# Optimization experiments

Measured on AMD Instinct MI355X. Metric: run time of the kernel, lower is better.

Reference implementation:

```python
import jax, jax.numpy as jnp
import numpy as np
from jax import lax

B, T, D = 2048, 300, 40
H = 64          # BasicLSTMCell num_units
D1 = 128        # dense1 units
OUT = 512       # out_dim (num speakers)
FORGET_BIAS = 1.0
BN_EPS = 1e-3   # tf.layers.BatchNormalization default


def setup_inputs() -> dict:
    key = jax.random.key(0)
    ks = jax.random.split(key, 10)
    X = jax.random.normal(ks[0], (B, T, D), dtype=jnp.float32)
    seq_length = jax.random.randint(ks[1], (B,), 1, T + 1).astype(jnp.int32)
    # BasicLSTMCell kernel: [input_dim + H, 4H], gate order i, j, f, o
    lstm_kernel = jax.random.normal(ks[2], (D + H, 4 * H), dtype=jnp.float32) * 0.08
    lstm_bias = jnp.zeros((4 * H,), dtype=jnp.float32)
    W1 = jax.random.normal(ks[3], (H, D1), dtype=jnp.float32) * 0.1
    b1 = jnp.zeros((D1,), dtype=jnp.float32)
    gamma = jnp.ones((D1,), dtype=jnp.float32)
    beta = jnp.zeros((D1,), dtype=jnp.float32)
    moving_mean = jnp.zeros((D1,), dtype=jnp.float32)
    moving_var = jnp.ones((D1,), dtype=jnp.float32)
    W2 = jax.random.normal(ks[4], (D1, OUT), dtype=jnp.float32) * 0.1
    b2 = jnp.zeros((OUT,), dtype=jnp.float32)
    return {"X": X, "seq_length": seq_length,
            "lstm_kernel": lstm_kernel, "lstm_bias": lstm_bias,
            "W1": W1, "b1": b1, "gamma": gamma, "beta": beta,
            "moving_mean": moving_mean, "moving_var": moving_var,
            "W2": W2, "b2": b2}


def reference(X, seq_length, lstm_kernel, lstm_bias, W1, b1, gamma, beta,
              moving_mean, moving_var, W2, b2):
    b = X.shape[0]
    c0 = jnp.zeros((b, H), dtype=X.dtype)
    h0 = jnp.zeros((b, H), dtype=X.dtype)

    def step(carry, x_t):
        c, h = carry
        z = jnp.concatenate([x_t, h], axis=1) @ lstm_kernel + lstm_bias
        i, j, f, o = jnp.split(z, 4, axis=1)
        new_c = c * jax.nn.sigmoid(f + FORGET_BIAS) + jax.nn.sigmoid(i) * jnp.tanh(j)
        new_h = jnp.tanh(new_c) * jax.nn.sigmoid(o)
        return (new_c, new_h), new_h

    _, outs = lax.scan(step, (c0, h0), jnp.swapaxes(X, 0, 1))  # [T, B, H]
    outs = jnp.swapaxes(outs, 0, 1)  # [B, T, H]

    # gather last valid timestep per sample
    idx = (seq_length - 1).astype(jnp.int32)
    final = jnp.take_along_axis(outs, idx[:, None, None], axis=1)[:, 0, :]  # [B, H]

    x = jax.nn.relu(final @ W1 + b1)
    # BatchNorm in inference mode (training=False): use moving statistics
    x = gamma * (x - moving_mean) * lax.rsqrt(moving_var + BN_EPS) + beta
    return jax.nn.softmax(x @ W2 + b2, axis=-1)
```

## Files before the change

### kernel.cpp

```cpp
#include <hip/hip_runtime.h>
#include <stdint.h>

#define TT 300
#define DD 40
#define SB 4
#define AROW 200
#define ABUF (16 * AROW)

typedef __attribute__((ext_vector_type(8))) short short8;
typedef __attribute__((ext_vector_type(4))) float f32x4;

__device__ __forceinline__ ushort f2bf(float f) {
  uint32_t b = __float_as_uint(f);
  b += 0x7FFFu + ((b >> 16) & 1u);
  return (ushort)(b >> 16);
}

__device__ __forceinline__ void bar() {
  asm volatile("s_waitcnt lgkmcnt(0)" ::: "memory");
  __builtin_amdgcn_s_barrier();
  asm volatile("" ::: "memory");
}

__global__ __launch_bounds__(256, 1) void lstm_mfma_kernel(
    const float* __restrict__ X, const int* __restrict__ seqlen,
    const float* __restrict__ Wk, const float* __restrict__ bias,
    float* __restrict__ hfin)
{
  __shared__ ushort wstage[64 * 192];
  __shared__ ushort Ash[2 * ABUF];

  const int tid = threadIdx.x;
  const int wv = tid >> 6, lane = tid & 63;
  const int s0 = blockIdx.x * SB;

  for (int i = tid; i < 2 * ABUF; i += 256) Ash[i] = 0;

  short8 Bf[6][4];
  for (int c = 0; c < 4; ++c) {
    __syncthreads();
    for (int i = tid; i < 64 * 192; i += 256) {
      int cc = i & 63, kp = i >> 6;
      int g = cc >> 4, u = c * 16 + (cc & 15);
      int col = g * 64 + u;
      ushort v = 0;
      if (kp < 40) {
        v = f2bf(Wk[kp * 256 + col]);
      } else if (kp < 42) {
        float bv = bias[col] + ((g == 2) ? 1.0f : 0.0f);
        ushort hi = f2bf(bv);
        v = (kp == 40) ? hi : f2bf(bv - __uint_as_float((uint32_t)hi << 16));
      } else if (kp >= 64) {
        v = f2bf(Wk[(40 + ((kp - 64) >> 1)) * 256 + col]);
      }
      wstage[cc * 192 + kp] = v;
    }
    __syncthreads();
    if (wv == c) {
      #pragma unroll
      for (int kt = 0; kt < 6; ++kt) {
        int kk = kt * 32 + (lane >> 4) * 8;
        #pragma unroll
        for (int g = 0; g < 4; ++g)
          Bf[kt][g] = *reinterpret_cast<const short8*>(
              &wstage[(g * 16 + (lane & 15)) * 192 + kk]);
      }
    }
  }

  const int u = wv * 16 + (lane & 15);
  const int q = lane >> 4;
  const bool act = (q < 2);
  const int sl0 = 2 * q, sl1 = sl0 + 1;
  const int len0 = seqlen[s0 + (sl0 & 3)], len1 = seqlen[s0 + (sl1 & 3)];

  int ml = seqlen[s0 + (lane & 3)];
  #pragma unroll
  for (int off = 1; off < 4; off <<= 1) ml = max(ml, __shfl_xor(ml, off));

  const bool hasX = (tid < SB * DD);
  const int sA = (tid * 205) >> 13, dA = tid - sA * 40;
  const int rA = 4 * (sA >> 1) + (sA & 1);
  const float* pA = X + (size_t)(s0 + sA) * (TT * DD) + dA;
  const int xiA = rA * AROW + dA;

  if (tid < 8) {
    int s = tid & 3, b = tid >> 2;
    int row = 4 * (s >> 1) + (s & 1);
    Ash[b * ABUF + row * AROW + 40] = 0x3F80;
    Ash[b * ABUF + row * AROW + 41] = 0x3F80;
  }
  float xv = 0.f;
  if (hasX) {
    Ash[xiA] = f2bf(pA[0]);
    if (ml > 1) xv = pA[DD];
  }
  __syncthreads();
  pA += 2 * DD;

  float c0 = 0.f, c1 = 0.f, hf0 = 0.f, hf1 = 0.f;
  int rb = 0, wb = ABUF;
  const int afb = (lane & 15) * AROW + q * 8;
  const int hw0 = (q * 4) * AROW + 64 + 2 * u;
  const int hw1 = (q * 4 + 1) * AROW + 64 + 2 * u;

  for (int t = 0; t < ml; ++t) {
    short8 Af[6];
    #pragma unroll
    for (int kt = 0; kt < 6; ++kt)
      Af[kt] = *reinterpret_cast<const short8*>(&Ash[rb + afb + kt * 32]);

    float xn = 0.f;
    if (hasX && t + 2 < ml) { xn = pA[0]; pA += DD; }

    f32x4 zero4 = {0.f, 0.f, 0.f, 0.f};
    f32x4 acc0 = zero4, acc1 = zero4, acc2 = zero4, acc3 = zero4;
    #pragma unroll
    for (int kt = 0; kt < 6; ++kt) {
      acc0 = __builtin_amdgcn_mfma_f32_16x16x32_bf16(Af[kt], Bf[kt][0], acc0, 0, 0, 0);
      acc1 = __builtin_amdgcn_mfma_f32_16x16x32_bf16(Af[kt], Bf[kt][1], acc1, 0, 0, 0);
      acc2 = __builtin_amdgcn_mfma_f32_16x16x32_bf16(Af[kt], Bf[kt][2], acc2, 0, 0, 0);
      acc3 = __builtin_amdgcn_mfma_f32_16x16x32_bf16(Af[kt], Bf[kt][3], acc3, 0, 0, 0);
    }

    if (act) {
      float Ef0 = __expf(-acc2[0]), Ei0 = __expf(-acc0[0]), Ej0 = __expf(2.f * acc1[0]);
      float nc0 = fmaf(c0, __builtin_amdgcn_rcpf(1.f + Ef0),
                       (Ej0 - 1.f) * __builtin_amdgcn_rcpf((1.f + Ei0) * (1.f + Ej0)));
      float En0 = __expf(2.f * fminf(nc0, 44.f)), Eo0 = __expf(-acc3[0]);
      float nh0 = (En0 - 1.f) * __builtin_amdgcn_rcpf((1.f + En0) * (1.f + Eo0));

      float Ef1 = __expf(-acc2[1]), Ei1 = __expf(-acc0[1]), Ej1 = __expf(2.f * acc1[1]);
      float nc1 = fmaf(c1, __builtin_amdgcn_rcpf(1.f + Ef1),
                       (Ej1 - 1.f) * __builtin_amdgcn_rcpf((1.f + Ei1) * (1.f + Ej1)));
      float En1 = __expf(2.f * fminf(nc1, 44.f)), Eo1 = __expf(-acc3[1]);
      float nh1 = (En1 - 1.f) * __builtin_amdgcn_rcpf((1.f + En1) * (1.f + Eo1));

      c0 = nc0; c1 = nc1;
      if (t == len0 - 1) hf0 = nh0;
      if (t == len1 - 1) hf1 = nh1;

      ushort hh0 = f2bf(nh0);
      ushort hl0 = f2bf(nh0 - __uint_as_float((uint32_t)hh0 << 16));
      ushort hh1 = f2bf(nh1);
      ushort hl1 = f2bf(nh1 - __uint_as_float((uint32_t)hh1 << 16));
      *reinterpret_cast<uint32_t*>(&Ash[wb + hw0]) = (uint32_t)hh0 | ((uint32_t)hl0 << 16);
      *reinterpret_cast<uint32_t*>(&Ash[wb + hw1]) = (uint32_t)hh1 | ((uint32_t)hl1 << 16);
    }
    if (hasX && t + 1 < ml) Ash[wb + xiA] = f2bf(xv);

    bar();
    rb ^= ABUF; wb ^= ABUF;
    xv = xn;
  }

  if (act) {
    hfin[(size_t)(s0 + sl0) * 64 + u] = hf0;
    hfin[(size_t)(s0 + sl1) * 64 + u] = hf1;
  }
}

__global__ __launch_bounds__(256, 1) void head_kernel(
    const float* __restrict__ hfin,
    const float* __restrict__ W1, const float* __restrict__ b1,
    const float* __restrict__ gamma, const float* __restrict__ beta,
    const float* __restrict__ mmean, const float* __restrict__ mvar,
    const float* __restrict__ W2, const float* __restrict__ b2,
    float* __restrict__ out)
{
  __shared__ float hl[16 * 64];
  __shared__ float d1t[128 * 20];
  __shared__ float lg[16 * 516];
  const int tid = threadIdx.x;
  const int b0 = blockIdx.x * 16;

  for (int i = tid; i < 16 * 64; i += 256) hl[i] = hfin[(size_t)b0 * 64 + i];
  __syncthreads();

  {
    const int j = tid & 127, sg = tid >> 7;
    float acc[8];
    const float bb = b1[j];
    #pragma unroll
    for (int s = 0; s < 8; ++s) acc[s] = bb;
    for (int k = 0; k < 64; ++k) {
      float w = W1[k * 128 + j];
      #pragma unroll
      for (int s = 0; s < 8; ++s) acc[s] = fmaf(hl[(sg * 8 + s) * 64 + k], w, acc[s]);
    }
    const float ga = gamma[j], be = beta[j], mm = mmean[j];
    const float iv = rsqrtf(mvar[j] + 1e-3f);
    #pragma unroll
    for (int s = 0; s < 8; ++s) {
      float v = fmaxf(acc[s], 0.f);
      d1t[j * 20 + sg * 8 + s] = ga * (v - mm) * iv + be;
    }
  }
  __syncthreads();

  {
    const int cA = tid * 2;
    float accA[16], accB[16];
    const float bA = b2[cA], bB = b2[cA + 1];
    #pragma unroll
    for (int s = 0; s < 16; ++s) { accA[s] = bA; accB[s] = bB; }
    for (int k = 0; k < 128; ++k) {
      const float2 w = *reinterpret_cast<const float2*>(&W2[k * 512 + cA]);
      const f32x4 dq0 = *reinterpret_cast<const f32x4*>(&d1t[k * 20]);
      const f32x4 dq1 = *reinterpret_cast<const f32x4*>(&d1t[k * 20 + 4]);
      const f32x4 dq2 = *reinterpret_cast<const f32x4*>(&d1t[k * 20 + 8]);
      const f32x4 dq3 = *reinterpret_cast<const f32x4*>(&d1t[k * 20 + 12]);
      #pragma unroll
      for (int s = 0; s < 4; ++s) {
        accA[s]      = fmaf(dq0[s], w.x, accA[s]);      accB[s]      = fmaf(dq0[s], w.y, accB[s]);
        accA[s + 4]  = fmaf(dq1[s], w.x, accA[s + 4]);  accB[s + 4]  = fmaf(dq1[s], w.y, accB[s + 4]);
        accA[s + 8]  = fmaf(dq2[s], w.x, accA[s + 8]);  accB[s + 8]  = fmaf(dq2[s], w.y, accB[s + 8]);
        accA[s + 12] = fmaf(dq3[s], w.x, accA[s + 12]); accB[s + 12] = fmaf(dq3[s], w.y, accB[s + 12]);
      }
    }
    #pragma unroll
    for (int s = 0; s < 16; ++s) {
      lg[s * 516 + cA]     = accA[s];
      lg[s * 516 + cA + 1] = accB[s];
    }
  }
  __syncthreads();

  {
    const int w = tid >> 6, lane = tid & 63;
    #pragma unroll
    for (int si = 0; si < 4; ++si) {
      const int s = w * 4 + si;
      float v[8];
      float m = -3.4e38f;
      #pragma unroll
      for (int i = 0; i < 8; ++i) { v[i] = lg[s * 516 + lane + 64 * i]; m = fmaxf(m, v[i]); }
      #pragma unroll
      for (int off = 1; off < 64; off <<= 1) m = fmaxf(m, __shfl_xor(m, off));
      float sum = 0.f;
      #pragma unroll
      for (int i = 0; i < 8; ++i) { v[i] = __expf(v[i] - m); sum += v[i]; }
      #pragma unroll
      for (int off = 1; off < 64; off <<= 1) sum += __shfl_xor(sum, off);
      const float inv = __builtin_amdgcn_rcpf(sum);
      #pragma unroll
      for (int i = 0; i < 8; ++i)
        out[(size_t)(b0 + s) * 512 + lane + 64 * i] = v[i] * inv;
    }
  }
}

extern "C" void kernel_launch(void* const* d_in, const int* in_sizes, int n_in,
                              void* d_out, int out_size, void* d_ws, size_t ws_size,
                              hipStream_t stream) {
  const float* X      = (const float*)d_in[0];
  const int*   seqlen = (const int*)d_in[1];
  const float* Wk     = (const float*)d_in[2];
  const float* bias   = (const float*)d_in[3];
  const float* W1     = (const float*)d_in[4];
  const float* b1     = (const float*)d_in[5];
  const float* gam    = (const float*)d_in[6];
  const float* bet    = (const float*)d_in[7];
  const float* mmean  = (const float*)d_in[8];
  const float* mvar   = (const float*)d_in[9];
  const float* W2     = (const float*)d_in[10];
  const float* b2     = (const float*)d_in[11];
  float* out  = (float*)d_out;
  float* hfin = (float*)d_ws;

  lstm_mfma_kernel<<<dim3(2048 / SB), dim3(256), 0, stream>>>(X, seqlen, Wk, bias, hfin);
  head_kernel<<<dim3(128), dim3(256), 0, stream>>>(hfin, W1, b1, gam, bet,
                                                   mmean, mvar, W2, b2, out);
}
```

Before: 425.7 us.

## Split LSTM gate tiles across 8 waves with 8 sequences per block

The recurrent MFMA kernel now runs 512 threads per block over 8 sequences, with each wave owning 8 hidden units and two gate n-tiles instead of four. The M dimension is now fully used, so no lanes sit idle in the activation math. Gate values are exchanged with lane shuffles. The A buffer gets an XOR-swizzled layout to avoid LDS bank conflicts, and the h-dependent MFMAs are issued before the x-dependent ones, with the x store moved earlier. The aim is to shorten the per-timestep critical path and raise occupancy, at the cost of more shuffles and twice as many waves meeting at each barrier.

```diff
diff --git a/kernel.cpp b/kernel.cpp
--- a/kernel.cpp
+++ b/kernel.cpp
@@ -3,9 +3,10 @@
 
 #define TT 300
 #define DD 40
-#define SB 4
-#define AROW 200
-#define ABUF (16 * AROW)
+#define SB 8
+#define AROWH 192
+#define ABYTES (16 * AROWH * 2)
+#define WROW 224
 
 typedef __attribute__((ext_vector_type(8))) short short8;
 typedef __attribute__((ext_vector_type(4))) float f32x4;
@@ -22,27 +23,31 @@
   asm volatile("" ::: "memory");
 }
 
-__global__ __launch_bounds__(256, 1) void lstm_mfma_kernel(
+__device__ __forceinline__ int aswz(int row, int colh) {
+  return ((row * AROWH + colh) * 2) ^ ((row & 7) << 4);
+}
+
+__global__ __launch_bounds__(512, 2) void lstm_mfma_kernel(
     const float* __restrict__ X, const int* __restrict__ seqlen,
     const float* __restrict__ Wk, const float* __restrict__ bias,
     float* __restrict__ hfin)
 {
-  __shared__ ushort wstage[64 * 192];
-  __shared__ ushort Ash[2 * ABUF];
+  __shared__ ushort shmem[64 * WROW];
+  char* const Ab = reinterpret_cast<char*>(shmem);
 
   const int tid = threadIdx.x;
   const int wv = tid >> 6, lane = tid & 63;
+  const int q = lane >> 4, n = lane & 15, m = n & 7, b = n >> 3;
   const int s0 = blockIdx.x * SB;
 
-  for (int i = tid; i < 2 * ABUF; i += 256) Ash[i] = 0;
-
-  short8 Bf[6][4];
+  short8 Bf[6][2];
   for (int c = 0; c < 4; ++c) {
-    __syncthreads();
-    for (int i = tid; i < 64 * 192; i += 256) {
+    for (int i = tid; i < 64 * 192; i += 512) {
       int cc = i & 63, kp = i >> 6;
-      int g = cc >> 4, u = c * 16 + (cc & 15);
-      int col = g * 64 + u;
+      int nb = cc & 15, nt = (cc >> 4) & 1, ws = cc >> 5;
+      int g = nt + 2 * (nb >> 3);
+      int uu = (2 * c + ws) * 8 + (nb & 7);
+      int col = g * 64 + uu;
       ushort v = 0;
       if (kp < 40) {
         v = f2bf(Wk[kp * 256 + col]);
@@ -53,111 +58,116 @@
       } else if (kp >= 64) {
         v = f2bf(Wk[(40 + ((kp - 64) >> 1)) * 256 + col]);
       }
-      wstage[cc * 192 + kp] = v;
+      shmem[cc * WROW + kp] = v;
     }
     __syncthreads();
-    if (wv == c) {
+    if ((wv >> 1) == c) {
+      const int cbase = (wv & 1) * 32;
       #pragma unroll
       for (int kt = 0; kt < 6; ++kt) {
-        int kk = kt * 32 + (lane >> 4) * 8;
         #pragma unroll
-        for (int g = 0; g < 4; ++g)
-          Bf[kt][g] = *reinterpret_cast<const short8*>(
-              &wstage[(g * 16 + (lane & 15)) * 192 + kk]);
+        for (int nt = 0; nt < 2; ++nt)
+          Bf[kt][nt] = *reinterpret_cast<const short8*>(
+              &shmem[(cbase + nt * 16 + n) * WROW + kt * 32 + q * 8]);
       }
     }
-  }
-
-  const int u = wv * 16 + (lane & 15);
-  const int q = lane >> 4;
-  const bool act = (q < 2);
-  const int sl0 = 2 * q, sl1 = sl0 + 1;
-  const int len0 = seqlen[s0 + (sl0 & 3)], len1 = seqlen[s0 + (sl1 & 3)];
-
-  int ml = seqlen[s0 + (lane & 3)];
+    __syncthreads();
+  }
+
+  for (int i = tid; i < 6144; i += 512) shmem[i] = 0;
+  __syncthreads();
+
+  const int u = wv * 8 + m;
+  const int sl = 2 * q + b;
+  const int len = seqlen[s0 + sl];
+  int ml = seqlen[s0 + (lane & 7)];
   #pragma unroll
-  for (int off = 1; off < 4; off <<= 1) ml = max(ml, __shfl_xor(ml, off));
+  for (int off = 1; off < 8; off <<= 1) ml = max(ml, __shfl_xor(ml, off));
 
   const bool hasX = (tid < SB * DD);
   const int sA = (tid * 205) >> 13, dA = tid - sA * 40;
   const int rA = 4 * (sA >> 1) + (sA & 1);
   const float* pA = X + (size_t)(s0 + sA) * (TT * DD) + dA;
-  const int xiA = rA * AROW + dA;
-
-  if (tid < 8) {
-    int s = tid & 3, b = tid >> 2;
+  const int xb = aswz(rA, dA);
+
+  if (tid < 16) {
+    int s = tid & 7, bb = tid >> 3;
     int row = 4 * (s >> 1) + (s & 1);
-    Ash[b * ABUF + row * AROW + 40] = 0x3F80;
-    Ash[b * ABUF + row * AROW + 41] = 0x3F80;
+    *reinterpret_cast<uint32_t*>(Ab + bb * ABYTES + aswz(row, 40)) = 0x3F803F80u;
   }
   float xv = 0.f;
   if (hasX) {
-    Ash[xiA] = f2bf(pA[0]);
+    *reinterpret_cast<ushort*>(Ab + xb) = f2bf(pA[0]);
     if (ml > 1) xv = pA[DD];
   }
   __syncthreads();
   pA += 2 * DD;
 
-  float c0 = 0.f, c1 = 0.f, hf0 = 0.f, hf1 = 0.f;
-  int rb = 0, wb = ABUF;
-  const int afb = (lane & 15) * AROW + q * 8;
-  const int hw0 = (q * 4) * AROW + 64 + 2 * u;
-  const int hw1 = (q * 4 + 1) * AROW + 64 + 2 * u;
+  int aoff[6];
+  #pragma unroll
+  for (int kt = 0; kt < 6; ++kt)
+    aoff[kt] = (n * 384 + kt * 64 + q * 16) ^ (m << 4);
+
+  float cst = 0.f, hf = 0.f;
+  int rb = 0, wb = ABYTES;
+  const int hb = aswz(4 * q + b, 64 + 2 * u);
 
   for (int t = 0; t < ml; ++t) {
-    short8 Af[6];
-    #pragma unroll
-    for (int kt = 0; kt < 6; ++kt)
-      Af[kt] = *reinterpret_cast<const short8*>(&Ash[rb + afb + kt * 32]);
-
+    short8 Ah[4];
+    #pragma unroll
+    for (int k2 = 0; k2 < 4; ++k2)
+      Ah[k2] = *reinterpret_cast<const short8*>(Ab + rb + aoff[k2 + 2]);
+
+    f32x4 zero4 = {0.f, 0.f, 0.f, 0.f};
+    f32x4 ah0 = zero4, ah1 = zero4;
+    #pragma unroll
+    for (int k2 = 0; k2 < 4; ++k2) {
+      ah0 = __builtin_amdgcn_mfma_f32_16x16x32_bf16(Ah[k2], Bf[k2 + 2][0], ah0, 0, 0, 0);
+      ah1 = __builtin_amdgcn_mfma_f32_16x16x32_bf16(Ah[k2], Bf[k2 + 2][1], ah1, 0, 0, 0);
+    }
+
+    short8 Ax0 = *reinterpret_cast<const short8*>(Ab + rb + aoff[0]);
+    short8 Ax1 = *reinterpret_cast<const short8*>(Ab + rb + aoff[1]);
+
+    if (hasX && t + 1 < ml) *reinterpret_cast<ushort*>(Ab + wb + xb) = f2bf(xv);
     float xn = 0.f;
     if (hasX && t + 2 < ml) { xn = pA[0]; pA += DD; }
 
-    f32x4 zero4 = {0.f, 0.f, 0.f, 0.f};
-    f32x4 acc0 = zero4, acc1 = zero4, acc2 = zero4, acc3 = zero4;
-    #pragma unroll
-    for (int kt = 0; kt < 6; ++kt) {
-      acc0 = __builtin_amdgcn_mfma_f32_16x16x32_bf16(Af[kt], Bf[kt][0], acc0, 0, 0, 0);
-      acc1 = __builtin_amdgcn_mfma_f32_16x16x32_bf16(Af[kt], Bf[kt][1], acc1, 0, 0, 0);
-      acc2 = __builtin_amdgcn_mfma_f32_16x16x32_bf16(Af[kt], Bf[kt][2], acc2, 0, 0, 0);
-      acc3 = __builtin_amdgcn_mfma_f32_16x16x32_bf16(Af[kt], Bf[kt][3], acc3, 0, 0, 0);
-    }
-
-    if (act) {
-      float Ef0 = __expf(-acc2[0]), Ei0 = __expf(-acc0[0]), Ej0 = __expf(2.f * acc1[0]);
-      float nc0 = fmaf(c0, __builtin_amdgcn_rcpf(1.f + Ef0),
-                       (Ej0 - 1.f) * __builtin_amdgcn_rcpf((1.f + Ei0) * (1.f + Ej0)));
-      float En0 = __expf(2.f * fminf(nc0, 44.f)), Eo0 = __expf(-acc3[0]);
-      float nh0 = (En0 - 1.f) * __builtin_amdgcn_rcpf((1.f + En0) * (1.f + Eo0));
-
-      float Ef1 = __expf(-acc2[1]), Ei1 = __expf(-acc0[1]), Ej1 = __expf(2.f * acc1[1]);
-      float nc1 = fmaf(c1, __builtin_amdgcn_rcpf(1.f + Ef1),
-                       (Ej1 - 1.f) * __builtin_amdgcn_rcpf((1.f + Ei1) * (1.f + Ej1)));
-      float En1 = __expf(2.f * fminf(nc1, 44.f)), Eo1 = __expf(-acc3[1]);
-      float nh1 = (En1 - 1.f) * __builtin_amdgcn_rcpf((1.f + En1) * (1.f + Eo1));
-
-      c0 = nc0; c1 = nc1;
-      if (t == len0 - 1) hf0 = nh0;
-      if (t == len1 - 1) hf1 = nh1;
-
-      ushort hh0 = f2bf(nh0);
-      ushort hl0 = f2bf(nh0 - __uint_as_float((uint32_t)hh0 << 16));
-      ushort hh1 = f2bf(nh1);
-      ushort hl1 = f2bf(nh1 - __uint_as_float((uint32_t)hh1 << 16));
-      *reinterpret_cast<uint32_t*>(&Ash[wb + hw0]) = (uint32_t)hh0 | ((uint32_t)hl0 << 16);
-      *reinterpret_cast<uint32_t*>(&Ash[wb + hw1]) = (uint32_t)hh1 | ((uint32_t)hl1 << 16);
-    }
-    if (hasX && t + 1 < ml) Ash[wb + xiA] = f2bf(xv);
+    f32x4 ax0 = zero4, ax1 = zero4;
+    ax0 = __builtin_amdgcn_mfma_f32_16x16x32_bf16(Ax0, Bf[0][0], ax0, 0, 0, 0);
+    ax1 = __builtin_amdgcn_mfma_f32_16x16x32_bf16(Ax0, Bf[0][1], ax1, 0, 0, 0);
+    ax0 = __builtin_amdgcn_mfma_f32_16x16x32_bf16(Ax1, Bf[1][0], ax0, 0, 0, 0);
+    ax1 = __builtin_amdgcn_mfma_f32_16x16x32_bf16(Ax1, Bf[1][1], ax1, 0, 0, 0);
+
+    f32x4 z0 = ah0 + ax0, z1 = ah1 + ax1;
+
+    float p00 = __shfl_xor(z0[0], 8);
+    float p01 = __shfl_xor(z0[1], 8);
+    float p10 = __shfl_xor(z1[0], 8);
+    float p11 = __shfl_xor(z1[1], 8);
+    float gi = b ? p01 : z0[0];
+    float gf = b ? z0[1] : p00;
+    float gj = b ? p11 : z1[0];
+    float go = b ? z1[1] : p10;
+
+    float Ef = __expf(-gf), Ei = __expf(-gi), Ej = __expf(2.f * gj);
+    float nc = fmaf(cst, __builtin_amdgcn_rcpf(1.f + Ef),
+                    (Ej - 1.f) * __builtin_amdgcn_rcpf((1.f + Ei) * (1.f + Ej)));
+    float En = __expf(2.f * fminf(nc, 44.f)), Eo = __expf(-go);
+    float nh = (En - 1.f) * __builtin_amdgcn_rcpf((1.f + En) * (1.f + Eo));
+    cst = nc;
+    if (t == len - 1) hf = nh;
+
+    ushort hh = (ushort)(__float_as_uint(nh) >> 16);
+    ushort hl = f2bf(nh - __uint_as_float((uint32_t)hh << 16));
+    *reinterpret_cast<uint32_t*>(Ab + wb + hb) = (uint32_t)hh | ((uint32_t)hl << 16);
 
     bar();
-    rb ^= ABUF; wb ^= ABUF;
+    rb ^= ABYTES; wb ^= ABYTES;
     xv = xn;
   }
 
-  if (act) {
-    hfin[(size_t)(s0 + sl0) * 64 + u] = hf0;
-    hfin[(size_t)(s0 + sl1) * 64 + u] = hf1;
-  }
+  hfin[(size_t)(s0 + sl) * 64 + u] = hf;
 }
 
 __global__ __launch_bounds__(256, 1) void head_kernel(
@@ -232,14 +242,14 @@
     for (int si = 0; si < 4; ++si) {
       const int s = w * 4 + si;
       float v[8];
-      float m = -3.4e38f;
-      #pragma unroll
-      for (int i = 0; i < 8; ++i) { v[i] = lg[s * 516 + lane + 64 * i]; m = fmaxf(m, v[i]); }
-      #pragma unroll
-      for (int off = 1; off < 64; off <<= 1) m = fmaxf(m, __shfl_xor(m, off));
+      float mx = -3.4e38f;
+      #pragma unroll
+      for (int i = 0; i < 8; ++i) { v[i] = lg[s * 516 + lane + 64 * i]; mx = fmaxf(mx, v[i]); }
+      #pragma unroll
+      for (int off = 1; off < 64; off <<= 1) mx = fmaxf(mx, __shfl_xor(mx, off));
       float sum = 0.f;
       #pragma unroll
-      for (int i = 0; i < 8; ++i) { v[i] = __expf(v[i] - m); sum += v[i]; }
+      for (int i = 0; i < 8; ++i) { v[i] = __expf(v[i] - mx); sum += v[i]; }
       #pragma unroll
       for (int off = 1; off < 64; off <<= 1) sum += __shfl_xor(sum, off);
       const float inv = __builtin_amdgcn_rcpf(sum);
@@ -268,7 +278,7 @@
   float* out  = (float*)d_out;
   float* hfin = (float*)d_ws;
 
-  lstm_mfma_kernel<<<dim3(2048 / SB), dim3(256), 0, stream>>>(X, seqlen, Wk, bias, hfin);
+  lstm_mfma_kernel<<<dim3(2048 / SB), dim3(512), 0, stream>>>(X, seqlen, Wk, bias, hfin);
   head_kernel<<<dim3(128), dim3(256), 0, stream>>>(hfin, W1, b1, gam, bet,
                                                    mmean, mvar, W2, b2, out);
 }
```

New measurement: 365.0 us. 14.3% less time.
